# Optimization experiments

Measured on AMD Instinct MI355X. Metric: run time of the kernel, lower is better.

## Reference

```python
import jax, jax.numpy as jnp
import numpy as np

GROUPS = 32
EPS = 1e-5
N_HEADS = 4


def group_norm(x, w, b):
    # x: [B, C, T]; GroupNorm over (C/G, T) within each of G groups
    B, C, T = x.shape
    xg = x.reshape(B, GROUPS, (C // GROUPS) * T)
    mean = xg.mean(axis=-1, keepdims=True)
    var = xg.var(axis=-1, keepdims=True)
    xn = ((xg - mean) * jax.lax.rsqrt(var + EPS)).reshape(B, C, T)
    return xn * w[None, :, None] + b[None, :, None]


def setup_inputs() -> dict:
    key = jax.random.key(0)
    ks = jax.random.split(key, 5)
    B, C, H, W = 2, 256, 64, 64
    x = jax.random.normal(ks[0], (B, C, H, W), dtype=jnp.float32)
    norm_w = jnp.ones((C,), dtype=jnp.float32)
    norm_b = jnp.zeros((C,), dtype=jnp.float32)
    qkv_w = jax.random.normal(ks[1], (3 * C, C), dtype=jnp.float32) * (C ** -0.5)
    qkv_b = jax.random.normal(ks[2], (3 * C,), dtype=jnp.float32) * 0.02
    proj_w = jax.random.normal(ks[3], (C, C), dtype=jnp.float32) * (C ** -0.5)
    proj_b = jax.random.normal(ks[4], (C,), dtype=jnp.float32) * 0.02
    return {"x": x, "norm_w": norm_w, "norm_b": norm_b,
            "qkv_w": qkv_w, "qkv_b": qkv_b,
            "proj_w": proj_w, "proj_b": proj_b}


def reference(x, norm_w, norm_b, qkv_w, qkv_b, proj_w, proj_b):
    B, C, Hs, Ws = x.shape
    T = Hs * Ws
    xf = x.reshape(B, C, T)
    xn = group_norm(xf, norm_w, norm_b)
    # 1x1 conv1d == channel matmul: [3C,C] x [B,C,T] -> [B,3C,T]
    qkv = jnp.einsum('oc,bct->bot', qkv_w, xn) + qkv_b[None, :, None]
    ch = C // N_HEADS
    # legacy order: [B, H*3*ch, T] -> [B*H, 3*ch, T] -> split
    qkv_h = qkv.reshape(B * N_HEADS, 3 * ch, T)
    q, k, v = qkv_h[:, :ch], qkv_h[:, ch:2 * ch], qkv_h[:, 2 * ch:]
    scale = ch ** -0.25
    # full [B*H, T, T] score matrix, softmax in fp32 (faithful to source)
    weight = jnp.einsum('bct,bcs->bts', q * scale, k * scale)
    weight = jax.nn.softmax(weight.astype(jnp.float32), axis=-1).astype(qkv.dtype)
    a = jnp.einsum('bts,bcs->bct', weight, v).reshape(B, C, T)
    h = jnp.einsum('oc,bct->bot', proj_w, a) + proj_b[None, :, None]
    return (xf + h).reshape(B, C, Hs, Ws)
```

## Files before the change

### kernel.cpp

```cpp
#include <hip/hip_runtime.h>
#include <hip/hip_bf16.h>

#define B_    2
#define C_    256
#define T_    4096
#define GRP   32
#define CPG   8
#define NH    4
#define CH    64
#define K3C   768
#define SPLIT 4
#define GSL   8
#define LOG2E 1.4426950408889634f

typedef __attribute__((ext_vector_type(8))) short bf16x8;
typedef __attribute__((ext_vector_type(4))) float f32x4;

#if __has_builtin(__builtin_amdgcn_exp2f)
#define EXP2(x) __builtin_amdgcn_exp2f(x)
#else
#define EXP2(x) exp2f(x)
#endif

__device__ __forceinline__ unsigned pk2(float a, float b) {
    __hip_bfloat162 h = __float22bfloat162_rn(make_float2(a, b));
    union { __hip_bfloat162 h2; unsigned u; } cv; cv.h2 = h;
    return cv.u;
}
__device__ __forceinline__ float bf2f(unsigned short u) {
    return __uint_as_float((unsigned)u << 16);
}

__global__ __launch_bounds__(256) void cvt_kernel(
    const float* __restrict__ qw, const float* __restrict__ pw,
    unsigned short* __restrict__ qwb, unsigned short* __restrict__ pwb) {
    int i = blockIdx.x * 256 + threadIdx.x;
    const int n1 = K3C * C_ / 8;
    const float* src; unsigned short* dst;
    if (i < n1) { src = qw + 8 * i; dst = qwb + 8 * i; }
    else { int j = i - n1; src = pw + 8 * j; dst = pwb + 8 * j; }
    float4 a = *(const float4*)src;
    float4 b = *(const float4*)(src + 4);
    uint4 u;
    u.x = pk2(a.x, a.y); u.y = pk2(a.z, a.w);
    u.z = pk2(b.x, b.y); u.w = pk2(b.z, b.w);
    *(uint4*)dst = u;
}

__global__ __launch_bounds__(256) void gn_stats_kernel(
    const float* __restrict__ x, float* __restrict__ stat) {
    int bg = blockIdx.x, sl = blockIdx.y;
    const int SLN = CPG * T_ / GSL;
    const float* xp = x + (size_t)bg * CPG * T_ + (size_t)sl * SLN;
    int tid = threadIdx.x;

    float s = 0.f, s2 = 0.f;
    for (int i = tid * 4; i < SLN; i += 1024) {
        float4 v = *(const float4*)&xp[i];
        s  += (v.x + v.y) + (v.z + v.w);
        s2 += (v.x * v.x + v.y * v.y) + (v.z * v.z + v.w * v.w);
    }
    for (int off = 32; off > 0; off >>= 1) {
        s  += __shfl_down(s,  off);
        s2 += __shfl_down(s2, off);
    }
    __shared__ float rs[4], rs2[4];
    int wid = tid >> 6;
    if ((tid & 63) == 0) { rs[wid] = s; rs2[wid] = s2; }
    __syncthreads();
    if (tid == 0) {
        float a = (rs[0] + rs[1]) + (rs[2] + rs[3]);
        float a2 = (rs2[0] + rs2[1]) + (rs2[2] + rs2[3]);
        stat[(bg * GSL + sl) * 2]     = a;
        stat[(bg * GSL + sl) * 2 + 1] = a2;
    }
}

__global__ __launch_bounds__(256) void gn_apply_kernel(
    const float* __restrict__ x, const float* __restrict__ stat,
    const float* __restrict__ w, const float* __restrict__ b,
    unsigned short* __restrict__ xnT) {
    int bg = blockIdx.x, sl = blockIdx.y;
    int batch = bg / GRP, g = bg % GRP;
    const float* xp = x + (size_t)bg * CPG * T_;
    int tid = threadIdx.x;

    float s = 0.f, s2 = 0.f;
#pragma unroll
    for (int i = 0; i < GSL; ++i) {
        s  += stat[(bg * GSL + i) * 2];
        s2 += stat[(bg * GSL + i) * 2 + 1];
    }
    float inv_n = 1.f / (float)(CPG * T_);
    float mean = s * inv_n;
    float var  = s2 * inv_n - mean * mean;
    float inv  = rsqrtf(var + 1e-5f);

    float wv[8], bv[8];
#pragma unroll
    for (int j = 0; j < 8; j++) {
        float ww = w[g * CPG + j] * inv;
        wv[j] = ww;
        bv[j] = b[g * CPG + j] - mean * ww;
    }
    unsigned short* op = xnT + (size_t)batch * T_ * C_ + g * CPG;
    int t0 = sl * (T_ / GSL);
#pragma unroll
    for (int rep = 0; rep < 2; ++rep) {
        int t = t0 + rep * 256 + tid;
        float v[8];
#pragma unroll
        for (int j = 0; j < 8; j++) v[j] = xp[(size_t)j * T_ + t] * wv[j] + bv[j];
        uint4 u;
        u.x = pk2(v[0], v[1]); u.y = pk2(v[2], v[3]);
        u.z = pk2(v[4], v[5]); u.w = pk2(v[6], v[7]);
        *(uint4*)&op[(size_t)t * C_] = u;
    }
}

__global__ __launch_bounds__(256) void qkv_gemm_kernel(
    const unsigned short* __restrict__ Wb, const float* __restrict__ bias,
    const unsigned short* __restrict__ Xt, unsigned short* __restrict__ q_t,
    unsigned short* __restrict__ k_t, unsigned short* __restrict__ v_d) {
    int tb = blockIdx.x * 128;
    int by = blockIdx.y;
    int bz = blockIdx.z;
    int ob = by * 64;
    int tid = threadIdx.x;
    int l = tid & 15, oct = (tid >> 4) & 3, w = tid >> 6;

    __shared__ __align__(16) unsigned short SH[64 * 264];

#pragma unroll
    for (int j = 0; j < 8; ++j) {
        int idx = tid + 256 * j;
        int row = idx >> 5, ch = idx & 31;
        *(uint4*)&SH[row * 264 + ch * 8] =
            *(const uint4*)&Wb[(size_t)(ob + row) * C_ + ch * 8];
    }
    __syncthreads();

    const unsigned short* Xb = Xt + (size_t)bz * T_ * C_;

    f32x4 acc[4][2];
#pragma unroll
    for (int mf = 0; mf < 4; ++mf)
#pragma unroll
        for (int nf = 0; nf < 2; ++nf) acc[mf][nf] = (f32x4){0.f, 0.f, 0.f, 0.f};

#pragma unroll
    for (int kk = 0; kk < 8; ++kk) {
        int c0 = 32 * kk + 8 * oct;
        bf16x8 bfr[2];
#pragma unroll
        for (int nf = 0; nf < 2; ++nf)
            bfr[nf] = *(const bf16x8*)&Xb[(size_t)(tb + 32 * w + 16 * nf + l) * C_ + c0];
#pragma unroll
        for (int mf = 0; mf < 4; ++mf) {
            bf16x8 af = *(const bf16x8*)&SH[(16 * mf + l) * 264 + c0];
#pragma unroll
            for (int nf = 0; nf < 2; ++nf)
                acc[mf][nf] = __builtin_amdgcn_mfma_f32_16x16x32_bf16(af, bfr[nf], acc[mf][nf], 0, 0, 0);
        }
    }

    int head = by / 3, sec = by - 3 * head;
    int bh = bz * NH + head;

    if (sec < 2) {
        float scale = (sec == 0) ? 0.125f * LOG2E : 1.f;
        unsigned short* dst = ((sec == 0) ? q_t : k_t) + (size_t)bh * T_ * CH;
#pragma unroll
        for (int mf = 0; mf < 4; ++mf) {
            float bvs[4];
#pragma unroll
            for (int r = 0; r < 4; ++r) bvs[r] = bias[ob + 16 * mf + 4 * oct + r];
#pragma unroll
            for (int nf = 0; nf < 2; ++nf) {
                int t = tb + 32 * w + 16 * nf + l;
                float v0 = (acc[mf][nf][0] + bvs[0]) * scale;
                float v1 = (acc[mf][nf][1] + bvs[1]) * scale;
                float v2 = (acc[mf][nf][2] + bvs[2]) * scale;
                float v3 = (acc[mf][nf][3] + bvs[3]) * scale;
                uint2 u; u.x = pk2(v0, v1); u.y = pk2(v2, v3);
                *(uint2*)&dst[(size_t)t * CH + 16 * mf + 4 * oct] = u;
            }
        }
    } else {
        __syncthreads();
#pragma unroll
        for (int mf = 0; mf < 4; ++mf) {
            float bvs[4];
#pragma unroll
            for (int r = 0; r < 4; ++r) bvs[r] = bias[ob + 16 * mf + 4 * oct + r];
#pragma unroll
            for (int nf = 0; nf < 2; ++nf) {
                int tl = 32 * w + 16 * nf + l;
#pragma unroll
                for (int r = 0; r < 4; ++r) {
                    unsigned pv = pk2(acc[mf][nf][r] + bvs[r], 0.f);
                    SH[(16 * mf + 4 * oct + r) * 136 + tl] = (unsigned short)(pv & 0xffffu);
                }
            }
        }
        __syncthreads();
        unsigned short* vdst = v_d + (size_t)bh * CH * T_;
#pragma unroll
        for (int j = 0; j < 4; ++j) {
            int idx = tid + 256 * j;
            int row = idx >> 4, ch = idx & 15;
            *(uint4*)&vdst[(size_t)row * T_ + tb + ch * 8] =
                *(uint4*)&SH[row * 136 + ch * 8];
        }
    }
}

__global__ __launch_bounds__(256, 4) void attn_kernel(
    const unsigned short* __restrict__ q_t, const unsigned short* __restrict__ k_t,
    const unsigned short* __restrict__ v_d, unsigned short* __restrict__ Opart,
    float* __restrict__ lbuf) {
    int bh = blockIdx.y;
    int sp = blockIdx.z;
    int t0 = blockIdx.x * 128;
    int tid = threadIdx.x;
    int l = tid & 15, q = (tid >> 4) & 3, w = tid >> 6;

    __shared__ __align__(16) unsigned short Kt[64][72];
    __shared__ __align__(16) unsigned short Vt[64][72];
    __shared__ __align__(16) unsigned short Ps[128][72];

    const unsigned short* qb = q_t + (size_t)bh * T_ * CH;
    const unsigned short* kb = k_t + (size_t)bh * T_ * CH;
    const unsigned short* vb = v_d + (size_t)bh * CH * T_;

    bf16x8 qf[2][2];
#pragma unroll
    for (int nf = 0; nf < 2; ++nf) {
        int t = t0 + 32 * w + 16 * nf + l;
#pragma unroll
        for (int kk = 0; kk < 2; ++kk)
            qf[nf][kk] = *(const bf16x8*)&qb[(size_t)t * CH + 32 * kk + 8 * q];
    }

    f32x4 O[4][2];
#pragma unroll
    for (int mf = 0; mf < 4; ++mf)
#pragma unroll
        for (int nf = 0; nf < 2; ++nf) O[mf][nf] = (f32x4){0.f, 0.f, 0.f, 0.f};
    float l_run[2] = {0.f, 0.f};

    int s_beg = sp * (T_ / SPLIT);
    int s_end = s_beg + (T_ / SPLIT);
    for (int s0 = s_beg; s0 < s_end; s0 += 64) {
#pragma unroll
        for (int it = 0; it < 2; ++it) {
            int row = (tid >> 3) + 32 * it;
            int ch  = tid & 7;
            *(uint4*)&Kt[row][ch * 8] =
                *(const uint4*)&kb[(size_t)(s0 + row) * CH + ch * 8];
            *(uint4*)&Vt[row][ch * 8] =
                *(const uint4*)&vb[(size_t)row * T_ + s0 + ch * 8];
        }
        __syncthreads();

        f32x4 S[4][2];
#pragma unroll
        for (int sf = 0; sf < 4; ++sf) {
            f32x4 a0 = (f32x4){0.f, 0.f, 0.f, 0.f};
            f32x4 a1 = (f32x4){0.f, 0.f, 0.f, 0.f};
#pragma unroll
            for (int kk = 0; kk < 2; ++kk) {
                bf16x8 ka = *(const bf16x8*)&Kt[16 * sf + l][32 * kk + 8 * q];
                a0 = __builtin_amdgcn_mfma_f32_16x16x32_bf16(ka, qf[0][kk], a0, 0, 0, 0);
                a1 = __builtin_amdgcn_mfma_f32_16x16x32_bf16(ka, qf[1][kk], a1, 0, 0, 0);
            }
            S[sf][0] = a0; S[sf][1] = a1;
        }

#pragma unroll
        for (int nf = 0; nf < 2; ++nf) {
            int trow = 32 * w + 16 * nf + l;
            float lloc = 0.f;
#pragma unroll
            for (int sf = 0; sf < 4; ++sf) {
                float p0 = EXP2(S[sf][nf][0]);
                float p1 = EXP2(S[sf][nf][1]);
                float p2 = EXP2(S[sf][nf][2]);
                float p3 = EXP2(S[sf][nf][3]);
                lloc += (p0 + p1) + (p2 + p3);
                uint2 u; u.x = pk2(p0, p1); u.y = pk2(p2, p3);
                *(uint2*)&Ps[trow][16 * sf + 4 * q] = u;
            }
            l_run[nf] += lloc;
        }

#pragma unroll
        for (int kk = 0; kk < 2; ++kk) {
            bf16x8 pb[2];
#pragma unroll
            for (int nf = 0; nf < 2; ++nf)
                pb[nf] = *(const bf16x8*)&Ps[32 * w + 16 * nf + l][32 * kk + 8 * q];
#pragma unroll
            for (int mf = 0; mf < 4; ++mf) {
                bf16x8 va = *(const bf16x8*)&Vt[16 * mf + l][32 * kk + 8 * q];
#pragma unroll
                for (int nf = 0; nf < 2; ++nf)
                    O[mf][nf] = __builtin_amdgcn_mfma_f32_16x16x32_bf16(va, pb[nf], O[mf][nf], 0, 0, 0);
            }
        }
        __syncthreads();
    }

#pragma unroll
    for (int nf = 0; nf < 2; ++nf) {
        float lt = l_run[nf];
        lt += __shfl_xor(lt, 16);
        lt += __shfl_xor(lt, 32);
        float inv = 1.f / lt;
        int t = t0 + 32 * w + 16 * nf + l;
        size_t row = (size_t)(sp * 8 + bh) * T_ + t;
        unsigned short* op = Opart + row * CH;
#pragma unroll
        for (int mf = 0; mf < 4; ++mf) {
            uint2 u;
            u.x = pk2(O[mf][nf][0] * inv, O[mf][nf][1] * inv);
            u.y = pk2(O[mf][nf][2] * inv, O[mf][nf][3] * inv);
            *(uint2*)&op[16 * mf + 4 * q] = u;
        }
        if (q == 0) lbuf[row] = lt;
    }
}

__global__ __launch_bounds__(256) void combine_kernel(
    const unsigned short* __restrict__ Opart, const float* __restrict__ lbuf,
    unsigned short* __restrict__ a_t) {
    int bx = blockIdx.x;
    int bh = bx >> 6;
    int tblk = bx & 63;
    int tid = threadIdx.x;
    int t = tblk * 64 + (tid >> 2);
    int sub = tid & 3;

    float lw[SPLIT];
    size_t rows[SPLIT];
    float lsum = 0.f;
#pragma unroll
    for (int sp = 0; sp < SPLIT; ++sp) {
        rows[sp] = (size_t)(sp * 8 + bh) * T_ + t;
        lw[sp] = lbuf[rows[sp]];
        lsum += lw[sp];
    }
    float inv = 1.f / lsum;

    float o[16];
#pragma unroll
    for (int i = 0; i < 16; ++i) o[i] = 0.f;
#pragma unroll
    for (int sp = 0; sp < SPLIT; ++sp) {
        float s = lw[sp] * inv;
        const unsigned short* p = Opart + rows[sp] * CH + sub * 16;
        uint4 u0 = *(const uint4*)p;
        uint4 u1 = *(const uint4*)(p + 8);
        unsigned us[8] = {u0.x, u0.y, u0.z, u0.w, u1.x, u1.y, u1.z, u1.w};
#pragma unroll
        for (int j = 0; j < 8; ++j) {
            o[2 * j]     += bf2f((unsigned short)(us[j] & 0xffffu)) * s;
            o[2 * j + 1] += bf2f((unsigned short)(us[j] >> 16)) * s;
        }
    }

    int batch = bh >> 2, h = bh & 3;
    unsigned short* dst = a_t + ((size_t)batch * T_ + t) * C_ + h * CH + sub * 16;
    uint4 u0, u1;
    u0.x = pk2(o[0], o[1]);   u0.y = pk2(o[2], o[3]);
    u0.z = pk2(o[4], o[5]);   u0.w = pk2(o[6], o[7]);
    u1.x = pk2(o[8], o[9]);   u1.y = pk2(o[10], o[11]);
    u1.z = pk2(o[12], o[13]); u1.w = pk2(o[14], o[15]);
    *(uint4*)dst = u0;
    *(uint4*)(dst + 8) = u1;
}

__global__ __launch_bounds__(256) void proj_gemm_kernel(
    const unsigned short* __restrict__ Wb, const float* __restrict__ bias,
    const unsigned short* __restrict__ At, const float* __restrict__ xres,
    float* __restrict__ out) {
    int tb = blockIdx.x * 128;
    int ob = blockIdx.y * 64;
    int bz = blockIdx.z;
    int tid = threadIdx.x;
    int l = tid & 15, oct = (tid >> 4) & 3, w = tid >> 6;

    __shared__ __align__(16) unsigned short SH[64 * 264];

#pragma unroll
    for (int j = 0; j < 8; ++j) {
        int idx = tid + 256 * j;
        int row = idx >> 5, ch = idx & 31;
        *(uint4*)&SH[row * 264 + ch * 8] =
            *(const uint4*)&Wb[(size_t)(ob + row) * C_ + ch * 8];
    }
    __syncthreads();

    const unsigned short* Ab = At + (size_t)bz * T_ * C_;

    f32x4 acc[4][2];
#pragma unroll
    for (int mf = 0; mf < 4; ++mf)
#pragma unroll
        for (int nf = 0; nf < 2; ++nf) acc[mf][nf] = (f32x4){0.f, 0.f, 0.f, 0.f};

#pragma unroll
    for (int kk = 0; kk < 8; ++kk) {
        int c0 = 32 * kk + 8 * oct;
        bf16x8 bfr[2];
#pragma unroll
        for (int nf = 0; nf < 2; ++nf)
            bfr[nf] = *(const bf16x8*)&Ab[(size_t)(tb + 32 * w + 16 * nf + l) * C_ + c0];
#pragma unroll
        for (int mf = 0; mf < 4; ++mf) {
            bf16x8 af = *(const bf16x8*)&SH[(16 * mf + l) * 264 + c0];
#pragma unroll
            for (int nf = 0; nf < 2; ++nf)
                acc[mf][nf] = __builtin_amdgcn_mfma_f32_16x16x32_bf16(af, bfr[nf], acc[mf][nf], 0, 0, 0);
        }
    }

#pragma unroll
    for (int mf = 0; mf < 4; ++mf) {
#pragma unroll
        for (int nf = 0; nf < 2; ++nf) {
            int t = tb + 32 * w + 16 * nf + l;
#pragma unroll
            for (int r = 0; r < 4; ++r) {
                int o = ob + 16 * mf + 4 * oct + r;
                size_t idx = ((size_t)bz * C_ + o) * T_ + t;
                out[idx] = acc[mf][nf][r] + bias[o] + xres[idx];
            }
        }
    }
}

extern "C" void kernel_launch(void* const* d_in, const int* in_sizes, int n_in,
                              void* d_out, int out_size, void* d_ws, size_t ws_size,
                              hipStream_t stream) {
    const float* x      = (const float*)d_in[0];
    const float* norm_w = (const float*)d_in[1];
    const float* norm_b = (const float*)d_in[2];
    const float* qkv_w  = (const float*)d_in[3];
    const float* qkv_b  = (const float*)d_in[4];
    const float* proj_w = (const float*)d_in[5];
    const float* proj_b = (const float*)d_in[6];
    float* out = (float*)d_out;

    char* p = (char*)d_ws;
    unsigned short* xnT = (unsigned short*)p; p += (size_t)B_ * T_ * C_ * 2;
    unsigned short* qwb = (unsigned short*)p; p += (size_t)K3C * C_ * 2;
    unsigned short* pwb = (unsigned short*)p; p += (size_t)C_ * C_ * 2;
    unsigned short* q_t = (unsigned short*)p; p += (size_t)B_ * NH * T_ * CH * 2;
    unsigned short* k_t = (unsigned short*)p; p += (size_t)B_ * NH * T_ * CH * 2;
    unsigned short* v_d = (unsigned short*)p; p += (size_t)B_ * NH * T_ * CH * 2;
    unsigned short* Opart = (unsigned short*)p; p += (size_t)SPLIT * 8 * T_ * CH * 2;
    float* lbuf         = (float*)p;          p += (size_t)SPLIT * 8 * T_ * 4;
    unsigned short* a_t = (unsigned short*)p; p += (size_t)B_ * T_ * C_ * 2;
    float* stat         = (float*)p;          p += (size_t)B_ * GRP * GSL * 2 * 4;

    cvt_kernel<<<dim3(128), dim3(256), 0, stream>>>(qkv_w, proj_w, qwb, pwb);
    gn_stats_kernel<<<dim3(B_ * GRP, GSL), dim3(256), 0, stream>>>(x, stat);
    gn_apply_kernel<<<dim3(B_ * GRP, GSL), dim3(256), 0, stream>>>(
        x, stat, norm_w, norm_b, xnT);
    qkv_gemm_kernel<<<dim3(T_ / 128, 12, B_), dim3(256), 0, stream>>>(
        qwb, qkv_b, xnT, q_t, k_t, v_d);
    attn_kernel<<<dim3(T_ / 128, B_ * NH, SPLIT), dim3(256), 0, stream>>>(
        q_t, k_t, v_d, Opart, lbuf);
    combine_kernel<<<dim3(B_ * NH * (T_ / 64)), dim3(256), 0, stream>>>(Opart, lbuf, a_t);
    proj_gemm_kernel<<<dim3(T_ / 128, C_ / 64, B_), dim3(256), 0, stream>>>(
        pwb, proj_b, a_t, x, out);
}
```

Measured before the change: 152.5 us.

## Fuse split-attention combine into projection GEMM and merge pre-kernels

Merges the weight-conversion and group-norm statistics kernels into one launch, and removes the separate combine kernel by having the projection GEMM read the split attention partials and merge them on the fly. This removes two kernel launches and the write and re-read of the intermediate attention buffer. In exchange, each projection block recomputes the combine for its tile, across all four output-channel blocks, so partial loads and conversion arithmetic are repeated fourfold.

```diff
diff --git a/kernel.cpp b/kernel.cpp
--- a/kernel.cpp
+++ b/kernel.cpp
@@ -31,48 +31,48 @@
     return __uint_as_float((unsigned)u << 16);
 }
 
-__global__ __launch_bounds__(256) void cvt_kernel(
+__global__ __launch_bounds__(256) void pre_kernel(
+    const float* __restrict__ x, float* __restrict__ stat,
     const float* __restrict__ qw, const float* __restrict__ pw,
     unsigned short* __restrict__ qwb, unsigned short* __restrict__ pwb) {
-    int i = blockIdx.x * 256 + threadIdx.x;
-    const int n1 = K3C * C_ / 8;
-    const float* src; unsigned short* dst;
-    if (i < n1) { src = qw + 8 * i; dst = qwb + 8 * i; }
-    else { int j = i - n1; src = pw + 8 * j; dst = pwb + 8 * j; }
-    float4 a = *(const float4*)src;
-    float4 b = *(const float4*)(src + 4);
-    uint4 u;
-    u.x = pk2(a.x, a.y); u.y = pk2(a.z, a.w);
-    u.z = pk2(b.x, b.y); u.w = pk2(b.z, b.w);
-    *(uint4*)dst = u;
-}
-
-__global__ __launch_bounds__(256) void gn_stats_kernel(
-    const float* __restrict__ x, float* __restrict__ stat) {
-    int bg = blockIdx.x, sl = blockIdx.y;
-    const int SLN = CPG * T_ / GSL;
-    const float* xp = x + (size_t)bg * CPG * T_ + (size_t)sl * SLN;
+    int bid = blockIdx.x;
     int tid = threadIdx.x;
-
-    float s = 0.f, s2 = 0.f;
-    for (int i = tid * 4; i < SLN; i += 1024) {
-        float4 v = *(const float4*)&xp[i];
-        s  += (v.x + v.y) + (v.z + v.w);
-        s2 += (v.x * v.x + v.y * v.y) + (v.z * v.z + v.w * v.w);
-    }
-    for (int off = 32; off > 0; off >>= 1) {
-        s  += __shfl_down(s,  off);
-        s2 += __shfl_down(s2, off);
-    }
-    __shared__ float rs[4], rs2[4];
-    int wid = tid >> 6;
-    if ((tid & 63) == 0) { rs[wid] = s; rs2[wid] = s2; }
-    __syncthreads();
-    if (tid == 0) {
-        float a = (rs[0] + rs[1]) + (rs[2] + rs[3]);
-        float a2 = (rs2[0] + rs2[1]) + (rs2[2] + rs2[3]);
-        stat[(bg * GSL + sl) * 2]     = a;
-        stat[(bg * GSL + sl) * 2 + 1] = a2;
+    if (bid < B_ * GRP * GSL) {
+        int bg = bid >> 3, sl = bid & 7;
+        const int SLN = CPG * T_ / GSL;
+        const float* xp = x + (size_t)bg * CPG * T_ + (size_t)sl * SLN;
+        float s = 0.f, s2 = 0.f;
+        for (int i = tid * 4; i < SLN; i += 1024) {
+            float4 v = *(const float4*)&xp[i];
+            s  += (v.x + v.y) + (v.z + v.w);
+            s2 += (v.x * v.x + v.y * v.y) + (v.z * v.z + v.w * v.w);
+        }
+        for (int off = 32; off > 0; off >>= 1) {
+            s  += __shfl_down(s,  off);
+            s2 += __shfl_down(s2, off);
+        }
+        __shared__ float rs[4], rs2[4];
+        int wid = tid >> 6;
+        if ((tid & 63) == 0) { rs[wid] = s; rs2[wid] = s2; }
+        __syncthreads();
+        if (tid == 0) {
+            float a = (rs[0] + rs[1]) + (rs[2] + rs[3]);
+            float a2 = (rs2[0] + rs2[1]) + (rs2[2] + rs2[3]);
+            stat[bid * 2]     = a;
+            stat[bid * 2 + 1] = a2;
+        }
+    } else {
+        int i = (bid - B_ * GRP * GSL) * 256 + tid;
+        const int n1 = K3C * C_ / 8;
+        const float* src; unsigned short* dst;
+        if (i < n1) { src = qw + 8 * i; dst = qwb + 8 * i; }
+        else { int j = i - n1; src = pw + 8 * j; dst = pwb + 8 * j; }
+        float4 a = *(const float4*)src;
+        float4 b = *(const float4*)(src + 4);
+        uint4 u;
+        u.x = pk2(a.x, a.y); u.y = pk2(a.z, a.w);
+        u.z = pk2(b.x, b.y); u.w = pk2(b.z, b.w);
+        *(uint4*)dst = u;
     }
 }
 
@@ -331,59 +331,10 @@
     }
 }
 
-__global__ __launch_bounds__(256) void combine_kernel(
-    const unsigned short* __restrict__ Opart, const float* __restrict__ lbuf,
-    unsigned short* __restrict__ a_t) {
-    int bx = blockIdx.x;
-    int bh = bx >> 6;
-    int tblk = bx & 63;
-    int tid = threadIdx.x;
-    int t = tblk * 64 + (tid >> 2);
-    int sub = tid & 3;
-
-    float lw[SPLIT];
-    size_t rows[SPLIT];
-    float lsum = 0.f;
-#pragma unroll
-    for (int sp = 0; sp < SPLIT; ++sp) {
-        rows[sp] = (size_t)(sp * 8 + bh) * T_ + t;
-        lw[sp] = lbuf[rows[sp]];
-        lsum += lw[sp];
-    }
-    float inv = 1.f / lsum;
-
-    float o[16];
-#pragma unroll
-    for (int i = 0; i < 16; ++i) o[i] = 0.f;
-#pragma unroll
-    for (int sp = 0; sp < SPLIT; ++sp) {
-        float s = lw[sp] * inv;
-        const unsigned short* p = Opart + rows[sp] * CH + sub * 16;
-        uint4 u0 = *(const uint4*)p;
-        uint4 u1 = *(const uint4*)(p + 8);
-        unsigned us[8] = {u0.x, u0.y, u0.z, u0.w, u1.x, u1.y, u1.z, u1.w};
-#pragma unroll
-        for (int j = 0; j < 8; ++j) {
-            o[2 * j]     += bf2f((unsigned short)(us[j] & 0xffffu)) * s;
-            o[2 * j + 1] += bf2f((unsigned short)(us[j] >> 16)) * s;
-        }
-    }
-
-    int batch = bh >> 2, h = bh & 3;
-    unsigned short* dst = a_t + ((size_t)batch * T_ + t) * C_ + h * CH + sub * 16;
-    uint4 u0, u1;
-    u0.x = pk2(o[0], o[1]);   u0.y = pk2(o[2], o[3]);
-    u0.z = pk2(o[4], o[5]);   u0.w = pk2(o[6], o[7]);
-    u1.x = pk2(o[8], o[9]);   u1.y = pk2(o[10], o[11]);
-    u1.z = pk2(o[12], o[13]); u1.w = pk2(o[14], o[15]);
-    *(uint4*)dst = u0;
-    *(uint4*)(dst + 8) = u1;
-}
-
 __global__ __launch_bounds__(256) void proj_gemm_kernel(
     const unsigned short* __restrict__ Wb, const float* __restrict__ bias,
-    const unsigned short* __restrict__ At, const float* __restrict__ xres,
-    float* __restrict__ out) {
+    const unsigned short* __restrict__ Opart, const float* __restrict__ lbuf,
+    const float* __restrict__ xres, float* __restrict__ out) {
     int tb = blockIdx.x * 128;
     int ob = blockIdx.y * 64;
     int bz = blockIdx.z;
@@ -399,9 +350,25 @@
         *(uint4*)&SH[row * 264 + ch * 8] =
             *(const uint4*)&Wb[(size_t)(ob + row) * C_ + ch * 8];
     }
+
+    float wgt[2][NH][SPLIT];
+#pragma unroll
+    for (int nf = 0; nf < 2; ++nf) {
+        int t = tb + 32 * w + 16 * nf + l;
+#pragma unroll
+        for (int h = 0; h < NH; ++h) {
+            float lw[SPLIT], lsum = 0.f;
+#pragma unroll
+            for (int sp = 0; sp < SPLIT; ++sp) {
+                lw[sp] = lbuf[(size_t)(sp * 8 + bz * NH + h) * T_ + t];
+                lsum += lw[sp];
+            }
+            float inv = 1.f / lsum;
+#pragma unroll
+            for (int sp = 0; sp < SPLIT; ++sp) wgt[nf][h][sp] = lw[sp] * inv;
+        }
+    }
     __syncthreads();
-
-    const unsigned short* Ab = At + (size_t)bz * T_ * C_;
 
     f32x4 acc[4][2];
 #pragma unroll
@@ -412,10 +379,32 @@
 #pragma unroll
     for (int kk = 0; kk < 8; ++kk) {
         int c0 = 32 * kk + 8 * oct;
+        int h  = c0 >> 6;
+        int ch0 = c0 & 63;
         bf16x8 bfr[2];
 #pragma unroll
-        for (int nf = 0; nf < 2; ++nf)
-            bfr[nf] = *(const bf16x8*)&Ab[(size_t)(tb + 32 * w + 16 * nf + l) * C_ + c0];
+        for (int nf = 0; nf < 2; ++nf) {
+            int t = tb + 32 * w + 16 * nf + l;
+            float o_[8];
+#pragma unroll
+            for (int i = 0; i < 8; ++i) o_[i] = 0.f;
+#pragma unroll
+            for (int sp = 0; sp < SPLIT; ++sp) {
+                size_t row = (size_t)(sp * 8 + bz * NH + h) * T_ + t;
+                uint4 u = *(const uint4*)&Opart[row * CH + ch0];
+                float s = wgt[nf][h][sp];
+                unsigned us[4] = {u.x, u.y, u.z, u.w};
+#pragma unroll
+                for (int j = 0; j < 4; ++j) {
+                    o_[2 * j]     += bf2f((unsigned short)(us[j] & 0xffffu)) * s;
+                    o_[2 * j + 1] += bf2f((unsigned short)(us[j] >> 16)) * s;
+                }
+            }
+            union { bf16x8 v; unsigned u[4]; } cv;
+            cv.u[0] = pk2(o_[0], o_[1]); cv.u[1] = pk2(o_[2], o_[3]);
+            cv.u[2] = pk2(o_[4], o_[5]); cv.u[3] = pk2(o_[6], o_[7]);
+            bfr[nf] = cv.v;
+        }
 #pragma unroll
         for (int mf = 0; mf < 4; ++mf) {
             bf16x8 af = *(const bf16x8*)&SH[(16 * mf + l) * 264 + c0];
@@ -461,18 +450,16 @@
     unsigned short* v_d = (unsigned short*)p; p += (size_t)B_ * NH * T_ * CH * 2;
     unsigned short* Opart = (unsigned short*)p; p += (size_t)SPLIT * 8 * T_ * CH * 2;
     float* lbuf         = (float*)p;          p += (size_t)SPLIT * 8 * T_ * 4;
-    unsigned short* a_t = (unsigned short*)p; p += (size_t)B_ * T_ * C_ * 2;
     float* stat         = (float*)p;          p += (size_t)B_ * GRP * GSL * 2 * 4;
 
-    cvt_kernel<<<dim3(128), dim3(256), 0, stream>>>(qkv_w, proj_w, qwb, pwb);
-    gn_stats_kernel<<<dim3(B_ * GRP, GSL), dim3(256), 0, stream>>>(x, stat);
+    pre_kernel<<<dim3(B_ * GRP * GSL + 128), dim3(256), 0, stream>>>(
+        x, stat, qkv_w, proj_w, qwb, pwb);
     gn_apply_kernel<<<dim3(B_ * GRP, GSL), dim3(256), 0, stream>>>(
         x, stat, norm_w, norm_b, xnT);
     qkv_gemm_kernel<<<dim3(T_ / 128, 12, B_), dim3(256), 0, stream>>>(
         qwb, qkv_b, xnT, q_t, k_t, v_d);
     attn_kernel<<<dim3(T_ / 128, B_ * NH, SPLIT), dim3(256), 0, stream>>>(
         q_t, k_t, v_d, Opart, lbuf);
-    combine_kernel<<<dim3(B_ * NH * (T_ / 64)), dim3(256), 0, stream>>>(Opart, lbuf, a_t);
     proj_gemm_kernel<<<dim3(T_ / 128, C_ / 64, B_), dim3(256), 0, stream>>>(
-        pwb, proj_b, a_t, x, out);
-}
+        pwb, proj_b, Opart, lbuf, x, out);
+}
```

Result: slower. 169.5 us (+11.1%).
